# Performance work log

Measured on AMD Instinct MI355X. Metric: run time of the kernel, lower is better.

The kernel has to match this reference:

```python
import jax, jax.numpy as jnp
import numpy as np

RES = 28          # resolution (H == W)
DIM = 384         # channels
NH = 8            # num_heads
HD = DIM // NH    # head_dim = 48
N = RES * RES     # tokens = 784
B = 16            # batch


def _build_bias_idxs(res):
    # Faithful reproduction of the first-occurrence offset indexing in __init__.
    pts = [(i, j) for i in range(res) for j in range(res)]
    offs = {}
    idxs = []
    for p1 in pts:
        for p2 in pts:
            o = (abs(p1[0] - p2[0]), abs(p1[1] - p2[1]))
            if o not in offs:
                offs[o] = len(offs)
            idxs.append(offs[o])
    return np.asarray(idxs, dtype=np.int32).reshape(res * res, res * res), len(offs)


def setup_inputs() -> dict:
    key = jax.random.key(0)
    ks = jax.random.split(key, 6)
    idxs, noff = _build_bias_idxs(RES)  # noff == RES*RES == 784
    s = 0.02
    return {
        "ll": jax.random.normal(ks[0], (B, DIM, RES, RES), jnp.float32),
        "high_attn": jax.random.normal(ks[1], (B, DIM, RES, RES), jnp.float32),
        # 1x1 convs stored as [out_ch, in_ch] matrices
        "q_w": jax.random.normal(ks[2], (DIM, DIM), jnp.float32) * s,
        "q_b": jnp.zeros((DIM,), jnp.float32),
        "kv_w": jax.random.normal(ks[3], (2 * DIM, DIM), jnp.float32) * s,
        "kv_b": jnp.zeros((2 * DIM,), jnp.float32),
        "proj_w": jax.random.normal(ks[4], (DIM, DIM), jnp.float32) * s,
        "proj_b": jnp.zeros((DIM,), jnp.float32),
        "attn_biases": jax.random.normal(ks[5], (NH, noff), jnp.float32) * s,
        "bias_idxs": jnp.asarray(idxs),  # [N, N] int32
    }


def reference(ll, high_attn, q_w, q_b, kv_w, kv_b, proj_w, proj_b, attn_biases, bias_idxs):
    b, c, h, w = ll.shape
    n = h * w
    scale = HD ** -0.5
    # 1x1 convs == per-pixel channel matmuls
    q = jnp.einsum('bchw,oc->bohw', ll, q_w) + q_b[:, None, None]
    kv = jnp.einsum('bchw,oc->bohw', high_attn, kv_w) + kv_b[:, None, None]
    k, v = jnp.split(kv, 2, axis=1)
    q = q.reshape(b, NH, HD, n).transpose(0, 1, 3, 2)  # [B,H,N,hd]
    k = k.reshape(b, NH, HD, n)                        # [B,H,hd,N]
    v = v.reshape(b, NH, HD, n).transpose(0, 1, 3, 2)  # [B,H,N,hd]
    attn = jnp.einsum('bhnd,bhdm->bhnm', q, k) * scale  # [B,H,N,N]
    bias = attn_biases[:, bias_idxs]                    # gather -> [H,N,N]
    attn = jax.nn.softmax(attn + bias[None], axis=-1)
    out = jnp.einsum('bhnm,bhmd->bhnd', attn, v)        # [B,H,N,hd]
    out = out.transpose(0, 1, 3, 2).reshape(b, c, h, w)
    return jnp.einsum('bchw,oc->bohw', out, proj_w) + proj_b[:, None, None]
```

## Files before the change

kernel.cpp:

```cpp
#include <hip/hip_runtime.h>

#define RES    28
#define DIMC   384
#define NHEAD  8
#define HDIM   48
#define DPAD   64
#define NPIX   784
#define NB     16
#define SC2    0.20823294f
#define LOG2E  1.44269504f

typedef short bf16x8 __attribute__((ext_vector_type(8)));
typedef float f32x4  __attribute__((ext_vector_type(4)));

__device__ __forceinline__ short f2bf(float x) {
  union { float f; unsigned u; } v; v.f = x;
  return (short)((v.u + 0x7FFFu + ((v.u >> 16) & 1u)) >> 16);
}
__device__ __forceinline__ unsigned pk_rne(float a, float b) {
  union { float f; unsigned u; } x, y; x.f = a; y.f = b;
  return __builtin_amdgcn_perm(y.u + 0x7FFFu + ((y.u >> 16) & 1u),
                               x.u + 0x7FFFu + ((x.u >> 16) & 1u), 0x07060302u);
}
__device__ __forceinline__ unsigned cvtpk(float a, float b) {
  unsigned r;
  asm("v_cvt_pk_bf16_f32 %0, %1, %2" : "=v"(r) : "v"(a), "v"(b));
  return r;
}
__device__ __forceinline__ float blo(unsigned u) { union { unsigned u; float f; } v; v.u = u << 16; return v.f; }
__device__ __forceinline__ float bhi(unsigned u) { union { unsigned u; float f; } v; v.u = u & 0xFFFF0000u; return v.f; }


__global__ __launch_bounds__(256) void prep_kernel(
    const float* __restrict__ ll, const float* __restrict__ ha,
    const float* __restrict__ qw, const float* __restrict__ kvw, const float* __restrict__ pw,
    const float* __restrict__ biases,
    short* __restrict__ Xll, short* __restrict__ Xha,
    short* __restrict__ Wf2, short* __restrict__ Wfp,
    short* __restrict__ Bt3, short* __restrict__ Qb,
    short* __restrict__ Kf, short* __restrict__ Vf)
{
  __shared__ __align__(16) short sT[64][72];
  __shared__ float sB[NPIX];
  const int bid = blockIdx.x, t = threadIdx.x;

  if (bid < 2496) {
    const int px = bid % 13, cb = (bid / 13) % 6, zz = bid / 78;
    const int which = zz >> 4, b = zz & 15;
    const float* X = (which ? ha : ll) + (size_t)b * DIMC * NPIX;
    short* T = (which ? Xha : Xll);
    const int c0 = cb * 64, p0 = px * 64;
    const int rrr = t >> 4, pc = (t & 15) * 4;
#pragma unroll
    for (int i = 0; i < 4; ++i) {
      const int c = rrr + 16 * i;
      if (p0 + pc < NPIX) {
        float4 v = *(const float4*)(X + (size_t)(c0 + c) * NPIX + p0 + pc);
        sT[pc + 0][c] = f2bf(v.x); sT[pc + 1][c] = f2bf(v.y);
        sT[pc + 2][c] = f2bf(v.z); sT[pc + 3][c] = f2bf(v.w);
      }
    }
    __syncthreads();
    const int rr = t & 15, qq = (t >> 4) & 3, w = t >> 6;
    const int pxt0 = p0 >> 4, ks0 = c0 >> 5;
#pragma unroll
    for (int i = 0; i < 2; ++i) {
      const int o = w * 2 + i;
      const int pxl = o >> 1, ksl = o & 1;
      if (pxt0 + pxl < 49) {
        short* dst = T + ((size_t)(b * 49 + pxt0 + pxl) * 12 + ks0 + ksl) * 512 + (t & 63) * 8;
        *(bf16x8*)dst = *(const bf16x8*)&sT[pxl * 16 + rr][ksl * 32 + qq * 8];
      }
    }
  } else if (bid < 2784) {
    int gid = (bid - 2496) * 256 + t;
    if (gid < 55296) {
      const int lane = gid & 63;
      const int mt = (gid >> 6) & 7;
      const int ks = (gid >> 9) % 12;
      const int ct = gid / 6144;
      const int chg = ct * 128 + mt * 16 + (lane & 15);
      const int k = ks * 32 + (lane >> 4) * 8;
      const float* src = (chg < DIMC ? qw + (size_t)chg * DIMC
                                     : kvw + (size_t)(chg - DIMC) * DIMC) + k;
      const float4 a = *(const float4*)src;
      const float4 b = *(const float4*)(src + 4);
      bf16x8 o;
      o[0] = f2bf(a.x); o[1] = f2bf(a.y); o[2] = f2bf(a.z); o[3] = f2bf(a.w);
      o[4] = f2bf(b.x); o[5] = f2bf(b.y); o[6] = f2bf(b.z); o[7] = f2bf(b.w);
      *(bf16x8*)(Wf2 + (size_t)gid * 8) = o;
    } else {
      const int g2 = gid - 55296;
      const int lane = g2 & 63;
      const int ks = (g2 >> 6) % 12;
      const int mtile = g2 / 768;
      const int row = mtile * 16 + (lane & 15);
      const int k = ks * 32 + (lane >> 4) * 8;
      const float* src = pw + (size_t)row * DIMC + k;
      const float4 a = *(const float4*)src;
      const float4 b = *(const float4*)(src + 4);
      bf16x8 o;
      o[0] = f2bf(a.x); o[1] = f2bf(a.y); o[2] = f2bf(a.z); o[3] = f2bf(a.w);
      o[4] = f2bf(b.x); o[5] = f2bf(b.y); o[6] = f2bf(b.z); o[7] = f2bf(b.w);
      *(bf16x8*)(Wfp + (size_t)g2 * 8) = o;
    }
  } else if (bid < 3176) {
    const int bb = bid - 2784;
    const int h = bb / 49, qt = bb % 49;
    for (int i = t; i < NPIX; i += 256) sB[i] = biases[h * NPIX + i] * LOG2E;
    __syncthreads();
    const int rr = t & 15, qq = (t >> 4) & 3, w = t >> 6;
    const int qrow = qt * 16 + rr;
    const int i2 = qrow / RES, j2 = qrow - i2 * RES;
    short* dst0 = Bt3 + ((size_t)(h * 49 + qt) * 25) * 512 + (t & 63) * 8;
    const short NEG = f2bf(-1e30f);
    for (int c = w; c < 25; c += 4) {
      short v8[8];
#pragma unroll
      for (int hf = 0; hf < 2; ++hf)
#pragma unroll
        for (int u = 0; u < 4; ++u) {
          const int k = c * 32 + hf * 16 + qq * 4 + u;
          if (k < NPIX) {
            const int i1 = k / RES, j1 = k - i1 * RES;
            int di = i1 - i2; di = di < 0 ? -di : di;
            int dj = j1 - j2; dj = dj < 0 ? -dj : dj;
            v8[hf * 4 + u] = f2bf(sB[di * RES + dj]);
          } else v8[hf * 4 + u] = NEG;
        }
      *(bf16x8*)(dst0 + (size_t)c * 512) = *(const bf16x8*)v8;
    }
  } else {
    const int pp = bid - 3176;
    if (pp < 392) {
      const size_t r = (size_t)pp * 256 + t;
      short* p = Qb + r * DPAD + HDIM;
      *(int4*)p = make_int4(0, 0, 0, 0);
      *(int4*)(p + 8) = make_int4(0, 0, 0, 0);
    } else if (pp < 1192) {
      const int id = (pp - 392) * 256 + t;
      const int l32 = id & 31;
      const int frag = 1 + 2 * ((id >> 5) & 1);
      const int chunk = (id >> 6) % 25;
      const int bh2 = id / 1600;
      short* dst = Kf + (((size_t)bh2 * 25 + chunk) * 4 + frag) * 512 + (32 + l32) * 8;
      *(int4*)dst = make_int4(0, 0, 0, 0);
    } else if (pp < 1256) {
      const int id = (pp - 1192) * 256 + t;
      const int lane2 = id & 63;
      const int frag = 2 + ((id >> 6) & 1);
      const int bh2 = id >> 7;
      short* dst = Kf + (((size_t)bh2 * 25 + 24) * 4 + frag) * 512 + lane2 * 8;
      *(int4*)dst = make_int4(0, 0, 0, 0);
    } else {
      const int id = (pp - 1256) * 256 + t;
      const int bh2 = id / 96;
      const int rem = id - bh2 * 96;
      const int frag = rem >> 5;
      const int l32 = rem & 31;
      short* dst = Vf + (((size_t)bh2 * 25 + 24) * 3 + frag) * 512 + (32 + l32) * 8;
      *(int4*)dst = make_int4(0, 0, 0, 0);
    }
  }
}

__global__ __launch_bounds__(256) void qkv_tiled(
    const short* __restrict__ Wf2, const float* __restrict__ qb, const float* __restrict__ kvb,
    const short* __restrict__ Xll, const short* __restrict__ Xha,
    short* __restrict__ Qb, short* __restrict__ Kf, short* __restrict__ Vf)
{
  __shared__ __align__(16) short sM[15360];
  const int t = threadIdx.x;
  const int w = t >> 6, lane = t & 63;
  const int rr = lane & 15, qq = lane >> 4;
  const int ct = blockIdx.x;
  const int pt = blockIdx.y;
  const int b = pt / 7, pt7 = pt % 7;
  const int px0 = pt7 * 112;

  const short* Xsel = (ct < 3 ? Xll : Xha);
  const int xt0 = b * 49 + pt7 * 7;

  const short* Ap = Wf2 + (size_t)ct * 12 * 4096 + 2 * w * 512 + lane * 8;

  f32x4 acc[2][7];
#pragma unroll
  for (int mi = 0; mi < 2; ++mi)
#pragma unroll
    for (int pg = 0; pg < 7; ++pg) acc[mi][pg] = (f32x4){0.f, 0.f, 0.f, 0.f};

  auto stageB = [&](int buf, int s) {
    short* l0 = &sM[buf * 3584 + w * 512];
    const short* g0 = Xsel + ((size_t)(xt0 + w) * 12 + s) * 512 + lane * 8;
    __builtin_amdgcn_global_load_lds((const __attribute__((address_space(1))) void*)g0,
                                     (__attribute__((address_space(3))) void*)l0, 16, 0, 0);
    if (w < 3) {
      short* l1 = &sM[buf * 3584 + (w + 4) * 512];
      const short* g1 = Xsel + ((size_t)(xt0 + w + 4) * 12 + s) * 512 + lane * 8;
      __builtin_amdgcn_global_load_lds((const __attribute__((address_space(1))) void*)g1,
                                       (__attribute__((address_space(3))) void*)l1, 16, 0, 0);
    }
  };

  stageB(0, 0);
  bf16x8 a0c = *(const bf16x8*)(Ap);
  bf16x8 a1c = *(const bf16x8*)(Ap + 512);
  __syncthreads();

  for (int s = 0; s < 12; ++s) {
    const int buf = s & 1;
    if (s < 11) stageB(buf ^ 1, s + 1);
    const int sn = s < 11 ? s + 1 : s;
    const short* an = Ap + (size_t)sn * 4096;
    const bf16x8 a0n = *(const bf16x8*)(an);
    const bf16x8 a1n = *(const bf16x8*)(an + 512);

    const short* sBb = &sM[buf * 3584];
#pragma unroll
    for (int pg = 0; pg < 7; ++pg) {
      const bf16x8 bf = *(const bf16x8*)(sBb + pg * 512 + lane * 8);
      acc[0][pg] = __builtin_amdgcn_mfma_f32_16x16x32_bf16(a0c, bf, acc[0][pg], 0, 0, 0);
      acc[1][pg] = __builtin_amdgcn_mfma_f32_16x16x32_bf16(a1c, bf, acc[1][pg], 0, 0, 0);
    }
    a0c = a0n; a1c = a1n;
    __syncthreads();
  }

  if (ct < 3) {
#pragma unroll
    for (int mi = 0; mi < 2; ++mi) {
      const int ch = ct * 128 + (2 * w + mi) * 16 + qq * 4;
      const float4 bv = *(const float4*)(qb + ch);
      const int hh = ch / HDIM, d0 = ch % HDIM;
#pragma unroll
      for (int pg = 0; pg < 7; ++pg) {
        const int px = px0 + pg * 16 + rr;
        uint2 pk;
        pk.x = pk_rne((acc[mi][pg][0] + bv.x) * SC2, (acc[mi][pg][1] + bv.y) * SC2);
        pk.y = pk_rne((acc[mi][pg][2] + bv.z) * SC2, (acc[mi][pg][3] + bv.w) * SC2);
        *(uint2*)(Qb + (((size_t)b * NHEAD + hh) * NPIX + px) * DPAD + d0) = pk;
      }
    }
  } else if (ct < 6) {
#pragma unroll
    for (int mi = 0; mi < 2; ++mi) {
      const int ch = (ct - 3) * 128 + (2 * w + mi) * 16 + qq * 4;
      const float4 bv = *(const float4*)(kvb + ch);
      const int hh = ch / HDIM, dq = ch % HDIM;
      const int fd = dq >> 5;
      const int laneHi = (dq & 31) >> 3;
      const int elo = dq & 7;
#pragma unroll
      for (int pg = 0; pg < 7; ++pg) {
        const int px = px0 + pg * 16 + rr;
        const int chunk = px >> 5, kh = (px >> 4) & 1;
        uint2 pk;
        pk.x = pk_rne(acc[mi][pg][0] + bv.x, acc[mi][pg][1] + bv.y);
        pk.y = pk_rne(acc[mi][pg][2] + bv.z, acc[mi][pg][3] + bv.w);
        short* dst = Kf + ((((size_t)b * NHEAD + hh) * 25 + chunk) * 4 + kh * 2 + fd) * 512
                     + ((px & 15) + (laneHi << 4)) * 8 + elo;
        *(uint2*)dst = pk;
      }
    }
  } else {
#pragma unroll
    for (int mi = 0; mi < 2; ++mi) {
      const int chl = (2 * w + mi) * 16 + qq * 4;
      const int chv = (ct - 6) * 128 + chl;
      const float4 bv = *(const float4*)(kvb + DIMC + chv);
      const float bb[4] = {bv.x, bv.y, bv.z, bv.w};
#pragma unroll
      for (int pg = 0; pg < 7; ++pg) {
        const int px = pg * 16 + rr;
#pragma unroll
        for (int j = 0; j < 4; ++j)
          sM[(chl + j) * 120 + px] = f2bf(acc[mi][pg][j] + bb[j]);
      }
    }
    __syncthreads();
    for (int id = t; id < 1792; id += 256) {
      const int r = id / 14, o = id - r * 14;
      const int k = px0 + o * 8;
      const int chunk = k >> 5, qv = (k >> 3) & 3;
      const int chv = (ct - 6) * 128 + r;
      const int hh = chv / HDIM, d = chv % HDIM;
      short* dst = Vf + ((((size_t)b * NHEAD + hh) * 25 + chunk) * 3 + (d >> 4)) * 512
                   + ((d & 15) + (qv << 4)) * 8;
      *(bf16x8*)dst = *(const bf16x8*)&sM[r * 120 + o * 8];
    }
  }
}

struct Chain { float sp; f32x4 O0, O1, O2; };

__device__ __forceinline__ void store_p(
    const f32x4 d0, const f32x4 d1, short* sPt, const int rr, const int qq)
{
  const float p0 = exp2f(d0[0]), p1 = exp2f(d0[1]), p2 = exp2f(d0[2]), p3 = exp2f(d0[3]);
  const float p4 = exp2f(d1[0]), p5 = exp2f(d1[1]), p6 = exp2f(d1[2]), p7 = exp2f(d1[3]);
  uint2 w0; w0.x = cvtpk(p0, p1); w0.y = cvtpk(p2, p3);
  uint2 w1; w1.x = cvtpk(p4, p5); w1.y = cvtpk(p6, p7);
  *(uint2*)(sPt + rr * 40 + qq * 4) = w0;
  *(uint2*)(sPt + rr * 40 + 16 + qq * 4) = w1;
}

__global__ __launch_bounds__(256) void attn_kernel(
    const short* __restrict__ Q, const short* __restrict__ Kf,
    const short* __restrict__ Vf, const short* __restrict__ Bt3,
    short* __restrict__ AOf)
{
  __shared__ __align__(16) char sMem[20480];
  short* sPbase = (short*)sMem;
  const int t = threadIdx.x;
  const int w = t >> 6, lane = t & 63;
  const int rr = lane & 15, qq = lane >> 4;
  const int x = blockIdx.x;
  const int h = x & 7;
  const int i = x >> 3;
  const int b = i / 25, qt = i - b * 25;
  const int qA = qt * 32;
  const bool hasB = (qA + 16 < NPIX);
  const int bh = b * NHEAD + h;

  const short* QpA = Q + ((size_t)bh * NPIX + qA + rr) * DPAD + qq * 8;
  const short* QpB = Q + ((size_t)bh * NPIX + (hasB ? qA + 16 : qA) + rr) * DPAD + qq * 8;
  const bf16x8 qfA0 = *(const bf16x8*)QpA;
  const bf16x8 qfA1 = *(const bf16x8*)(QpA + 32);
  const bf16x8 qfB0 = *(const bf16x8*)QpB;
  const bf16x8 qfB1 = *(const bf16x8*)(QpB + 32);

  const short* Kfp = Kf + (size_t)bh * (25 * 4 * 512) + lane * 8;
  const short* Vfp = Vf + (size_t)bh * (25 * 3 * 512) + lane * 8;
  const short* BpA = Bt3 + ((size_t)(h * 49 + 2 * qt) * 25) * 512 + lane * 8;
  const short* BpB = Bt3 + ((size_t)(h * 49 + (hasB ? 2 * qt + 1 : 2 * qt)) * 25) * 512 + lane * 8;
  short* sPA = sPbase + (w * 2 + 0) * 640;
  short* sPB = sPbase + (w * 2 + 1) * 640;

  const bf16x8 onesf = {(short)0x3F80, (short)0x3F80, (short)0x3F80, (short)0x3F80,
                        (short)0x3F80, (short)0x3F80, (short)0x3F80, (short)0x3F80};

  Chain cA, cB;
  cA.O0 = (f32x4){0.f,0.f,0.f,0.f}; cA.O1 = cA.O0; cA.O2 = cA.O0;
  cB.O0 = cA.O0; cB.O1 = cA.O0; cB.O2 = cA.O0;
  f32x4 spA = cA.O0, spB = cA.O0;

  const int cbeg = w * 6;
  const int cend = (w == 3) ? 25 : cbeg + 6;

  for (int c = cbeg; c < cend; ++c) {
    const uint4 bA = *(const uint4*)(BpA + (size_t)c * 512);
    const uint4 bB = *(const uint4*)(BpB + (size_t)c * 512);
    const short* kc = Kfp + (size_t)c * 2048;
    const bf16x8 ka0 = *(const bf16x8*)kc;
    const bf16x8 ka1 = *(const bf16x8*)(kc + 512);
    const bf16x8 kb0 = *(const bf16x8*)(kc + 1024);
    const bf16x8 kb1 = *(const bf16x8*)(kc + 1536);

    f32x4 dA0 = (f32x4){blo(bA.x), bhi(bA.x), blo(bA.y), bhi(bA.y)};
    f32x4 dA1 = (f32x4){blo(bA.z), bhi(bA.z), blo(bA.w), bhi(bA.w)};
    f32x4 dB0 = (f32x4){blo(bB.x), bhi(bB.x), blo(bB.y), bhi(bB.y)};
    f32x4 dB1 = (f32x4){blo(bB.z), bhi(bB.z), blo(bB.w), bhi(bB.w)};

    __builtin_amdgcn_s_setprio(1);
    dA0 = __builtin_amdgcn_mfma_f32_16x16x32_bf16(ka0, qfA0, dA0, 0, 0, 0);
    dA0 = __builtin_amdgcn_mfma_f32_16x16x32_bf16(ka1, qfA1, dA0, 0, 0, 0);
    dB0 = __builtin_amdgcn_mfma_f32_16x16x32_bf16(ka0, qfB0, dB0, 0, 0, 0);
    dB0 = __builtin_amdgcn_mfma_f32_16x16x32_bf16(ka1, qfB1, dB0, 0, 0, 0);
    dA1 = __builtin_amdgcn_mfma_f32_16x16x32_bf16(kb0, qfA0, dA1, 0, 0, 0);
    dA1 = __builtin_amdgcn_mfma_f32_16x16x32_bf16(kb1, qfA1, dA1, 0, 0, 0);
    dB1 = __builtin_amdgcn_mfma_f32_16x16x32_bf16(kb0, qfB0, dB1, 0, 0, 0);
    dB1 = __builtin_amdgcn_mfma_f32_16x16x32_bf16(kb1, qfB1, dB1, 0, 0, 0);
    __builtin_amdgcn_s_setprio(0);

    store_p(dA0, dA1, sPA, rr, qq);
    store_p(dB0, dB1, sPB, rr, qq);

    const short* vc = Vfp + (size_t)c * 1536;
    const bf16x8 vf0 = *(const bf16x8*)vc;
    const bf16x8 vf1 = *(const bf16x8*)(vc + 512);
    const bf16x8 vf2 = *(const bf16x8*)(vc + 1024);
    const bf16x8 pfA = *(const bf16x8*)(sPA + rr * 40 + qq * 8);
    const bf16x8 pfB = *(const bf16x8*)(sPB + rr * 40 + qq * 8);
    __builtin_amdgcn_s_setprio(1);
    cA.O0 = __builtin_amdgcn_mfma_f32_16x16x32_bf16(vf0, pfA, cA.O0, 0, 0, 0);
    cA.O1 = __builtin_amdgcn_mfma_f32_16x16x32_bf16(vf1, pfA, cA.O1, 0, 0, 0);
    cA.O2 = __builtin_amdgcn_mfma_f32_16x16x32_bf16(vf2, pfA, cA.O2, 0, 0, 0);
    spA   = __builtin_amdgcn_mfma_f32_16x16x32_bf16(onesf, pfA, spA, 0, 0, 0);
    cB.O0 = __builtin_amdgcn_mfma_f32_16x16x32_bf16(vf0, pfB, cB.O0, 0, 0, 0);
    cB.O1 = __builtin_amdgcn_mfma_f32_16x16x32_bf16(vf1, pfB, cB.O1, 0, 0, 0);
    cB.O2 = __builtin_amdgcn_mfma_f32_16x16x32_bf16(vf2, pfB, cB.O2, 0, 0, 0);
    spB   = __builtin_amdgcn_mfma_f32_16x16x32_bf16(onesf, pfB, spB, 0, 0, 0);
    __builtin_amdgcn_s_setprio(0);
  }
  cA.sp = spA[0];
  cB.sp = spB[0];

  __syncthreads();
  float* mbuf = (float*)sMem;
  if (w > 0) {
    const int col = ((w - 1) * 2 + 0) * 64 + lane;
    const int colB = col + 64;
    float vals[13] = {cA.O0[0], cA.O0[1], cA.O0[2], cA.O0[3],
                      cA.O1[0], cA.O1[1], cA.O1[2], cA.O1[3],
                      cA.O2[0], cA.O2[1], cA.O2[2], cA.O2[3], cA.sp};
    float valsB[13] = {cB.O0[0], cB.O0[1], cB.O0[2], cB.O0[3],
                       cB.O1[0], cB.O1[1], cB.O1[2], cB.O1[3],
                       cB.O2[0], cB.O2[1], cB.O2[2], cB.O2[3], cB.sp};
#pragma unroll
    for (int j = 0; j < 13; ++j) mbuf[j * 384 + col] = vals[j];
#pragma unroll
    for (int j = 0; j < 13; ++j) mbuf[j * 384 + colB] = valsB[j];
  }
  __syncthreads();
  if (w != 0) return;

#pragma unroll
  for (int ww = 0; ww < 3; ++ww) {
    const int col = (ww * 2 + 0) * 64 + lane;
    const int colB = col + 64;
#pragma unroll
    for (int j = 0; j < 4; ++j) {
      cA.O0[j] += mbuf[j * 384 + col];
      cA.O1[j] += mbuf[(4 + j) * 384 + col];
      cA.O2[j] += mbuf[(8 + j) * 384 + col];
      cB.O0[j] += mbuf[j * 384 + colB];
      cB.O1[j] += mbuf[(4 + j) * 384 + colB];
      cB.O2[j] += mbuf[(8 + j) * 384 + colB];
    }
    cA.sp += mbuf[12 * 384 + col];
    cB.sp += mbuf[12 * 384 + colB];
  }

  {
    const float invA = 1.f / cA.sp;
    const f32x4 OA[3] = {cA.O0, cA.O1, cA.O2};
    short* base = AOf + ((size_t)(b * 49 + 2 * qt) * 12) * 512;
#pragma unroll
    for (int part = 0; part < 3; ++part) {
      const int ch = h * HDIM + part * 16 + qq * 4;
      uint2 pk;
      pk.x = pk_rne(OA[part][0] * invA, OA[part][1] * invA);
      pk.y = pk_rne(OA[part][2] * invA, OA[part][3] * invA);
      short* dst = base + (ch >> 5) * 512 + (rr + (((ch >> 3) & 3) << 4)) * 8 + (ch & 7);
      *(uint2*)dst = pk;
    }
  }
  if (hasB) {
    const float invB = 1.f / cB.sp;
    const f32x4 OB[3] = {cB.O0, cB.O1, cB.O2};
    short* base = AOf + ((size_t)(b * 49 + 2 * qt + 1) * 12) * 512;
#pragma unroll
    for (int part = 0; part < 3; ++part) {
      const int ch = h * HDIM + part * 16 + qq * 4;
      uint2 pk;
      pk.x = pk_rne(OB[part][0] * invB, OB[part][1] * invB);
      pk.y = pk_rne(OB[part][2] * invB, OB[part][3] * invB);
      short* dst = base + (ch >> 5) * 512 + (rr + (((ch >> 3) & 3) << 4)) * 8 + (ch & 7);
      *(uint2*)dst = pk;
    }
  }
}

__global__ __launch_bounds__(256) void proj_gemm(
    const short* __restrict__ Wfp, const float* __restrict__ pb,
    const short* __restrict__ AOf, float* __restrict__ out)
{
  const int t = threadIdx.x;
  const int w = t >> 6, lane = t & 63;
  const int rr = lane & 15, qq = lane >> 4;
  const int b = blockIdx.y;
  const int bx = blockIdx.x;
  const int pix = bx * 16 + rr;

  const short* Xp = AOf + ((size_t)(b * 49 + bx) * 12) * 512 + lane * 8;
  const short* wfp = Wfp + ((size_t)w * 12 * 64 + lane) * 8;

  f32x4 acc[6];
#pragma unroll
  for (int i = 0; i < 6; ++i) acc[i] = (f32x4){0.f, 0.f, 0.f, 0.f};

  bf16x8 xfc = *(const bf16x8*)(Xp);
  bf16x8 afc[6];
#pragma unroll
  for (int i = 0; i < 6; ++i) afc[i] = *(const bf16x8*)(wfp + (size_t)i * 24576);

#pragma unroll 2
  for (int ks = 0; ks < 12; ++ks) {
    const int kn = ks + (ks < 11 ? 1 : 0);
    const bf16x8 xfn = *(const bf16x8*)(Xp + kn * 512);
    bf16x8 afn[6];
#pragma unroll
    for (int i = 0; i < 6; ++i)
      afn[i] = *(const bf16x8*)(wfp + (size_t)i * 24576 + kn * 512);

#pragma unroll
    for (int i = 0; i < 6; ++i)
      acc[i] = __builtin_amdgcn_mfma_f32_16x16x32_bf16(afc[i], xfc, acc[i], 0, 0, 0);

    xfc = xfn;
#pragma unroll
    for (int i = 0; i < 6; ++i) afc[i] = afn[i];
  }
#pragma unroll
  for (int i = 0; i < 6; ++i) {
    const int ch0 = (w + 4 * i) * 16 + qq * 4;
    const float4 bv = *(const float4*)(pb + ch0);
    float* o = out + ((size_t)b * DIMC + ch0) * NPIX + pix;
    o[0] = acc[i][0] + bv.x;
    o[NPIX] = acc[i][1] + bv.y;
    o[2 * NPIX] = acc[i][2] + bv.z;
    o[3 * NPIX] = acc[i][3] + bv.w;
  }
}

extern "C" void kernel_launch(void* const* d_in, const int* in_sizes, int n_in,
                              void* d_out, int out_size, void* d_ws, size_t ws_size,
                              hipStream_t stream)
{
  const float* ll     = (const float*)d_in[0];
  const float* ha     = (const float*)d_in[1];
  const float* q_w    = (const float*)d_in[2];
  const float* q_b    = (const float*)d_in[3];
  const float* kv_w   = (const float*)d_in[4];
  const float* kv_b   = (const float*)d_in[5];
  const float* proj_w = (const float*)d_in[6];
  const float* proj_b = (const float*)d_in[7];
  const float* biases = (const float*)d_in[8];
  float* out = (float*)d_out;

  short* Qb  = (short*)d_ws;
  short* Kf  = Qb  + (size_t)NB * NHEAD * NPIX * DPAD;
  short* Vf  = Kf  + (size_t)128 * 25 * 4 * 512;
  short* Xll = Vf  + (size_t)128 * 25 * 3 * 512;
  short* Xha = Xll + (size_t)NB * 49 * 12 * 512;
  short* AOf = Xha + (size_t)NB * 49 * 12 * 512;
  short* Bt3 = AOf + (size_t)NB * 49 * 12 * 512;
  short* Wf2 = Bt3 + (size_t)NHEAD * 49 * 25 * 512;
  short* Wfp = Wf2 + (size_t)55296 * 8;

  prep_kernel<<<dim3(4480), 256, 0, stream>>>(ll, ha, q_w, kv_w, proj_w, biases,
                                              Xll, Xha, Wf2, Wfp, Bt3, Qb, Kf, Vf);
  qkv_tiled<<<dim3(9, 112), 256, 0, stream>>>(Wf2, q_b, kv_b, Xll, Xha, Qb, Kf, Vf);
  attn_kernel<<<dim3(3200), 256, 0, stream>>>(Qb, Kf, Vf, Bt3, AOf);
  proj_gemm<<<dim3(49, NB), 256, 0, stream>>>(Wfp, proj_b, AOf, out);
}
```

Before: 194.8 us.

## Retile projection GEMM into 64-channel by 112-pixel blocks with register reuse

The output projection GEMM is retiled. Each 128-thread block now computes 64 output channels for 112 pixels, and each wave holds 2 weight fragments against 7 activation fragments, where before one 16-pixel column was computed against all 384 channels. This raises operand reuse per load, cutting redundant global reads of weight fragments across pixel blocks. The cost is more accumulator registers and a different grid shape, 672 blocks of 2 waves. The Wfp layout indexing is assumed to match the weight fragment order produced by prep_kernel.

```diff
diff --git a/kernel.cpp b/kernel.cpp
--- a/kernel.cpp
+++ b/kernel.cpp
@@ -461,55 +461,69 @@
   }
 }
 
-__global__ __launch_bounds__(256) void proj_gemm(
+__global__ __launch_bounds__(128) void proj_gemm(
     const short* __restrict__ Wfp, const float* __restrict__ pb,
     const short* __restrict__ AOf, float* __restrict__ out)
 {
   const int t = threadIdx.x;
   const int w = t >> 6, lane = t & 63;
   const int rr = lane & 15, qq = lane >> 4;
-  const int b = blockIdx.y;
-  const int bx = blockIdx.x;
-  const int pix = bx * 16 + rr;
-
-  const short* Xp = AOf + ((size_t)(b * 49 + bx) * 12) * 512 + lane * 8;
-  const short* wfp = Wfp + ((size_t)w * 12 * 64 + lane) * 8;
-
-  f32x4 acc[6];
-#pragma unroll
-  for (int i = 0; i < 6; ++i) acc[i] = (f32x4){0.f, 0.f, 0.f, 0.f};
-
-  bf16x8 xfc = *(const bf16x8*)(Xp);
-  bf16x8 afc[6];
-#pragma unroll
-  for (int i = 0; i < 6; ++i) afc[i] = *(const bf16x8*)(wfp + (size_t)i * 24576);
+  const int ct = blockIdx.x;
+  const int pt = blockIdx.y;
+  const int b = pt / 7, pt7 = pt % 7;
+  const int px0 = pt7 * 112;
+
+  const short* Ap0 = Wfp + ((size_t)(ct * 4 + 2 * w) * 12) * 512 + lane * 8;
+  const short* Ap1 = Ap0 + 12 * 512;
+  const short* Xp[7];
+#pragma unroll
+  for (int pg = 0; pg < 7; ++pg)
+    Xp[pg] = AOf + ((size_t)(b * 49 + pt7 * 7 + pg) * 12) * 512 + lane * 8;
+
+  f32x4 acc[2][7];
+#pragma unroll
+  for (int mi = 0; mi < 2; ++mi)
+#pragma unroll
+    for (int pg = 0; pg < 7; ++pg) acc[mi][pg] = (f32x4){0.f, 0.f, 0.f, 0.f};
+
+  bf16x8 a0c = *(const bf16x8*)(Ap0);
+  bf16x8 a1c = *(const bf16x8*)(Ap1);
+  bf16x8 bcur[7];
+#pragma unroll
+  for (int pg = 0; pg < 7; ++pg) bcur[pg] = *(const bf16x8*)(Xp[pg]);
 
 #pragma unroll 2
-  for (int ks = 0; ks < 12; ++ks) {
-    const int kn = ks + (ks < 11 ? 1 : 0);
-    const bf16x8 xfn = *(const bf16x8*)(Xp + kn * 512);
-    bf16x8 afn[6];
-#pragma unroll
-    for (int i = 0; i < 6; ++i)
-      afn[i] = *(const bf16x8*)(wfp + (size_t)i * 24576 + kn * 512);
-
-#pragma unroll
-    for (int i = 0; i < 6; ++i)
-      acc[i] = __builtin_amdgcn_mfma_f32_16x16x32_bf16(afc[i], xfc, acc[i], 0, 0, 0);
-
-    xfc = xfn;
-#pragma unroll
-    for (int i = 0; i < 6; ++i) afc[i] = afn[i];
-  }
-#pragma unroll
-  for (int i = 0; i < 6; ++i) {
-    const int ch0 = (w + 4 * i) * 16 + qq * 4;
+  for (int s = 0; s < 12; ++s) {
+    const int sn = s + (s < 11 ? 1 : 0);
+    const bf16x8 a0n = *(const bf16x8*)(Ap0 + (size_t)sn * 512);
+    const bf16x8 a1n = *(const bf16x8*)(Ap1 + (size_t)sn * 512);
+    bf16x8 bnxt[7];
+#pragma unroll
+    for (int pg = 0; pg < 7; ++pg) bnxt[pg] = *(const bf16x8*)(Xp[pg] + (size_t)sn * 512);
+
+#pragma unroll
+    for (int pg = 0; pg < 7; ++pg) {
+      acc[0][pg] = __builtin_amdgcn_mfma_f32_16x16x32_bf16(a0c, bcur[pg], acc[0][pg], 0, 0, 0);
+      acc[1][pg] = __builtin_amdgcn_mfma_f32_16x16x32_bf16(a1c, bcur[pg], acc[1][pg], 0, 0, 0);
+    }
+    a0c = a0n; a1c = a1n;
+#pragma unroll
+    for (int pg = 0; pg < 7; ++pg) bcur[pg] = bnxt[pg];
+  }
+
+#pragma unroll
+  for (int mi = 0; mi < 2; ++mi) {
+    const int ch0 = ct * 64 + (2 * w + mi) * 16 + qq * 4;
     const float4 bv = *(const float4*)(pb + ch0);
-    float* o = out + ((size_t)b * DIMC + ch0) * NPIX + pix;
-    o[0] = acc[i][0] + bv.x;
-    o[NPIX] = acc[i][1] + bv.y;
-    o[2 * NPIX] = acc[i][2] + bv.z;
-    o[3 * NPIX] = acc[i][3] + bv.w;
+#pragma unroll
+    for (int pg = 0; pg < 7; ++pg) {
+      const int px = px0 + pg * 16 + rr;
+      float* o = out + ((size_t)b * DIMC + ch0) * NPIX + px;
+      o[0] = acc[mi][pg][0] + bv.x;
+      o[NPIX] = acc[mi][pg][1] + bv.y;
+      o[2 * NPIX] = acc[mi][pg][2] + bv.z;
+      o[3 * NPIX] = acc[mi][pg][3] + bv.w;
+    }
   }
 }
 
@@ -542,5 +556,5 @@
                                               Xll, Xha, Wf2, Wfp, Bt3, Qb, Kf, Vf);
   qkv_tiled<<<dim3(9, 112), 256, 0, stream>>>(Wf2, q_b, kv_b, Xll, Xha, Qb, Kf, Vf);
   attn_kernel<<<dim3(3200), 256, 0, stream>>>(Qb, Kf, Vf, Bt3, AOf);
-  proj_gemm<<<dim3(49, NB), 256, 0, stream>>>(Wfp, proj_b, AOf, out);
-}
+  proj_gemm<<<dim3(6, 112), 128, 0, stream>>>(Wfp, proj_b, AOf, out);
+}
```

Result: no change. 193.3 us (median of 3 runs) (-0.7%).
